# Performance work log

Measured on AMD Instinct MI355X. Metric: run time of the kernel, lower is better.

The kernel has to match this reference:

```python
import jax, jax.numpy as jnp
import numpy as np

B, T, D, H = 2, 2048, 2048, 16
HD = D // H
EPS = 1e-8
NEG = -1e9


def setup_inputs() -> dict:
    key = jax.random.key(0)
    ks = jax.random.split(key, 6)
    x = jax.random.normal(ks[0], (B, T, D), dtype=jnp.float32)
    # additive causal mask, broadcast over [B, H, T, T]
    causal = jnp.tril(jnp.ones((T, T), dtype=bool))
    attn_mask = jnp.where(causal, 0.0, NEG).astype(jnp.float32)[None, None]
    s = 1.0 / np.sqrt(D)
    w_norm = jnp.ones((D,), dtype=jnp.float32)
    wq = jax.random.normal(ks[1], (D, D), dtype=jnp.float32) * s
    wk = jax.random.normal(ks[2], (D, D), dtype=jnp.float32) * s
    wv = jax.random.normal(ks[3], (D, D), dtype=jnp.float32) * s
    wo = jax.random.normal(ks[4], (D, D), dtype=jnp.float32) * s
    return {"x": x, "attn_mask": attn_mask, "w_norm": w_norm,
            "wq": wq, "wk": wk, "wv": wv, "wo": wo}


def _rmsnorm(x, w):
    # norm = ||x||_2 * D^-0.5 ; out = w * x / (norm + eps)  (eps outside, as in source)
    norm = jnp.sqrt(jnp.sum(x * x, axis=-1, keepdims=True)) * (x.shape[-1] ** -0.5)
    return w * x / (norm + EPS)


def reference(x, attn_mask, w_norm, wq, wk, wv, wo):
    b, t, d = x.shape
    xn = _rmsnorm(x, w_norm)
    # Linear (no bias): y = x @ W^T ; split into heads -> [B, H, T, HD]
    def proj(w):
        return jnp.einsum('btd,ed->bte', xn, w).reshape(b, t, H, HD).transpose(0, 2, 1, 3)
    q, k, v = proj(wq), proj(wk), proj(wv)
    scale = HD ** -0.5
    w_scores = jnp.einsum('bhqd,bhkd->bhqk', q, k) * scale + attn_mask
    p = jax.nn.softmax(w_scores, axis=-1)
    out = jnp.einsum('bhqk,bhkd->bhqd', p, v)
    out = out.transpose(0, 2, 1, 3).reshape(b, t, d)
    return jnp.einsum('btd,ed->bte', out, wo)
```

## Files before the change

### kernel.cpp

```cpp
#include <hip/hip_runtime.h>
#include <stdint.h>

#define TT 2048
#define DD 2048
#define NHH 16
#define HDD 128
#define BTT 4096

typedef __attribute__((ext_vector_type(8))) short bf16x8;
typedef __attribute__((ext_vector_type(4))) float f32x4;

#define MF(a, b, c) __builtin_amdgcn_mfma_f32_16x16x32_bf16(a, b, c, 0, 0, 0)

__device__ __forceinline__ unsigned short f2bf(float f) {
    union { float f; uint32_t u; } v; v.f = f;
    uint32_t u = v.u;
    u += 0x7fffu + ((u >> 16) & 1u);
    return (unsigned short)(u >> 16);
}

__device__ __forceinline__ void gld16(const unsigned short* g, unsigned short* l) {
    __builtin_amdgcn_global_load_lds(
        (const __attribute__((address_space(1))) unsigned int*)g,
        (__attribute__((address_space(3))) unsigned int*)l, 16, 0, 0);
}

__global__ __launch_bounds__(256) void convert_w(const float* __restrict__ wq,
                                                 const float* __restrict__ wk,
                                                 const float* __restrict__ wv,
                                                 const float* __restrict__ wo,
                                                 unsigned short* __restrict__ out) {
    size_t gid = (size_t)blockIdx.x * 256 + threadIdx.x;
    size_t base = gid * 8;
    int which = (int)(base >> 22);
    const float* src = which == 0 ? wq : which == 1 ? wk : which == 2 ? wv : wo;
    size_t off = base & 4194303u;
    float4 a = ((const float4*)(src + off))[0];
    float4 b = ((const float4*)(src + off))[1];
    union { unsigned short us[8]; uint4 v; } pk;
    pk.us[0] = f2bf(a.x); pk.us[1] = f2bf(a.y); pk.us[2] = f2bf(a.z); pk.us[3] = f2bf(a.w);
    pk.us[4] = f2bf(b.x); pk.us[5] = f2bf(b.y); pk.us[6] = f2bf(b.z); pk.us[7] = f2bf(b.w);
    *(uint4*)(out + base) = pk.v;
}

__global__ __launch_bounds__(256) void rmsnorm_k(const float* __restrict__ x,
                                                 const float* __restrict__ w,
                                                 unsigned short* __restrict__ xn) {
    const int row = blockIdx.x;
    const int tid = threadIdx.x;
    const float* xr = x + (size_t)row * DD;
    float4 a = ((const float4*)xr)[tid * 2];
    float4 b = ((const float4*)xr)[tid * 2 + 1];
    float ss = a.x*a.x + a.y*a.y + a.z*a.z + a.w*a.w
             + b.x*b.x + b.y*b.y + b.z*b.z + b.w*b.w;
    #pragma unroll
    for (int m = 1; m < 64; m <<= 1) ss += __shfl_xor(ss, m, 64);
    __shared__ float wss[4];
    if ((tid & 63) == 0) wss[tid >> 6] = ss;
    __syncthreads();
    float total = wss[0] + wss[1] + wss[2] + wss[3];
    float norm = sqrtf(total) * 0.022097086912079612f;
    float inv = 1.0f / (norm + 1e-8f);
    float4 wa = ((const float4*)w)[tid * 2];
    float4 wb = ((const float4*)w)[tid * 2 + 1];
    union { unsigned short us[8]; uint4 v; } pk;
    pk.us[0] = f2bf(wa.x * a.x * inv); pk.us[1] = f2bf(wa.y * a.y * inv);
    pk.us[2] = f2bf(wa.z * a.z * inv); pk.us[3] = f2bf(wa.w * a.w * inv);
    pk.us[4] = f2bf(wb.x * b.x * inv); pk.us[5] = f2bf(wb.y * b.y * inv);
    pk.us[6] = f2bf(wb.z * b.z * inv); pk.us[7] = f2bf(wb.w * b.w * inv);
    ((uint4*)(xn + (size_t)row * DD))[tid] = pk.v;
}

__device__ __forceinline__ void stage_tile(const unsigned short* __restrict__ Ag,
                                           const unsigned short* __restrict__ Bg,
                                           int k0, unsigned short* buf,
                                           int swA, int swB, size_t goff) {
    #pragma unroll
    for (int c = 0; c < 2; c++)
        gld16(Ag + (size_t)(swA + c * 8) * DD + k0 + goff, buf + (swA + c * 8) * 64);
    #pragma unroll
    for (int c = 0; c < 4; c++)
        gld16(Bg + (size_t)(swB + c * 8) * DD + k0 + goff, buf + 8192 + (swB + c * 8) * 64);
}

__device__ __forceinline__ void gemm128x256_core(const unsigned short* __restrict__ Ag,
                                                 const unsigned short* __restrict__ Bg,
                                                 unsigned short* lds, f32x4 acc[4][4]) {
    const int tid = threadIdx.x;
    const int wave = tid >> 6, lane = tid & 63;
    const int wm = wave >> 2, wn = wave & 3;
    const int l15 = lane & 15, lq = lane >> 4, r7 = l15 & 7;
    const int gr = lane >> 3;
    const size_t goff = (size_t)gr * DD + (size_t)(((lane & 7) ^ gr) * 8);
    const int xk0 = (lq ^ r7) * 8;
    const int xk1 = ((4 + lq) ^ r7) * 8;
    const int aro = (wm * 64 + l15) * 64;
    const int bro = 8192 + (wn * 64 + l15) * 64;
    const int swA = wave * 16;
    const int swB = wave * 32;
    unsigned short* p0 = lds;
    unsigned short* p1 = lds + 24576;
    unsigned short* p2 = lds + 49152;

    stage_tile(Ag, Bg, 0, p0, swA, swB, goff);
    stage_tile(Ag, Bg, 64, p1, swA, swB, goff);
    asm volatile("s_waitcnt vmcnt(6)" ::: "memory");
    __builtin_amdgcn_sched_barrier(0);
    __builtin_amdgcn_s_barrier();

    for (int kt = 0; kt < 32; kt++) {
        if (kt + 2 < 32)
            stage_tile(Ag, Bg, (kt + 2) * 64, p2, swA, swB, goff);
        const unsigned short* ac = p0 + aro;
        const unsigned short* bc = p0 + bro;
        bf16x8 a[4][2], b[4][2];
        #pragma unroll
        for (int m = 0; m < 4; m++) {
            a[m][0] = *(const bf16x8*)(ac + m * 1024 + xk0);
            a[m][1] = *(const bf16x8*)(ac + m * 1024 + xk1);
        }
        #pragma unroll
        for (int n = 0; n < 4; n++) {
            b[n][0] = *(const bf16x8*)(bc + n * 1024 + xk0);
            b[n][1] = *(const bf16x8*)(bc + n * 1024 + xk1);
        }
        asm volatile("s_waitcnt lgkmcnt(0)" ::: "memory");
        __builtin_amdgcn_sched_barrier(0);
        __builtin_amdgcn_s_setprio(1);
        #pragma unroll
        for (int m = 0; m < 4; m++)
            #pragma unroll
            for (int n = 0; n < 4; n++) {
                acc[m][n] = MF(a[m][0], b[n][0], acc[m][n]);
                acc[m][n] = MF(a[m][1], b[n][1], acc[m][n]);
            }
        __builtin_amdgcn_s_setprio(0);
        if (kt + 1 < 32) {
            if (kt + 2 < 32) { asm volatile("s_waitcnt vmcnt(6)" ::: "memory"); }
            else             { asm volatile("s_waitcnt vmcnt(0)" ::: "memory"); }
            __builtin_amdgcn_sched_barrier(0);
        }
        __builtin_amdgcn_s_barrier();
        unsigned short* t = p0; p0 = p1; p1 = p2; p2 = t;
    }
}

__global__ __launch_bounds__(512, 2) void gemm_qkv(const unsigned short* __restrict__ A,
                                                   const unsigned short* __restrict__ W3,
                                                   unsigned short* __restrict__ O3) {
    __shared__ __align__(16) unsigned short lds[73728];
    const int orig = blockIdx.y * 32 + blockIdx.x;
    const int id = (orig & 7) * 96 + (orig >> 3);
    const int which = id >> 8;
    const int rem = id & 255;
    const int bn = rem >> 5, bm = rem & 31;
    const unsigned short* Bw = W3 + (size_t)which * DD * DD;
    unsigned short* C = O3 + (size_t)which * BTT * DD;
    const int m0 = bm * 128, n0 = bn * 256;
    const f32x4 zf = {0.f, 0.f, 0.f, 0.f};
    f32x4 acc[4][4];
    #pragma unroll
    for (int m = 0; m < 4; m++)
        #pragma unroll
        for (int n = 0; n < 4; n++) acc[m][n] = zf;
    gemm128x256_core(A + (size_t)m0 * DD, Bw + (size_t)n0 * DD, lds, acc);
    const int wave = threadIdx.x >> 6, lane = threadIdx.x & 63;
    const int wm = wave >> 2, wn = wave & 3;
    const int l15 = lane & 15, lq = lane >> 4;
    #pragma unroll
    for (int m = 0; m < 4; m++) {
        const int row = m0 + wm * 64 + m * 16 + lq * 4;
        #pragma unroll
        for (int n = 0; n < 4; n++) {
            const int col = n0 + wn * 64 + n * 16 + l15;
            #pragma unroll
            for (int r = 0; r < 4; r++)
                C[(size_t)(row + r) * DD + col] = f2bf(acc[m][n][r]);
        }
    }
}

__global__ __launch_bounds__(512, 2) void gemm_out(const unsigned short* __restrict__ A,
                                                   const unsigned short* __restrict__ Bw,
                                                   float* __restrict__ C) {
    __shared__ __align__(16) unsigned short lds[73728];
    const int orig = blockIdx.y * 32 + blockIdx.x;
    const int id = (orig & 7) * 32 + (orig >> 3);
    const int bn = id >> 5, bm = id & 31;
    const int m0 = bm * 128, n0 = bn * 256;
    const f32x4 zf = {0.f, 0.f, 0.f, 0.f};
    f32x4 acc[4][4];
    #pragma unroll
    for (int m = 0; m < 4; m++)
        #pragma unroll
        for (int n = 0; n < 4; n++) acc[m][n] = zf;
    gemm128x256_core(A + (size_t)m0 * DD, Bw + (size_t)n0 * DD, lds, acc);
    const int wave = threadIdx.x >> 6, lane = threadIdx.x & 63;
    const int wm = wave >> 2, wn = wave & 3;
    const int l15 = lane & 15, lq = lane >> 4;
    #pragma unroll
    for (int m = 0; m < 4; m++) {
        const int row = m0 + wm * 64 + m * 16 + lq * 4;
        #pragma unroll
        for (int n = 0; n < 4; n++) {
            const int col = n0 + wn * 64 + n * 16 + l15;
            #pragma unroll
            for (int r = 0; r < 4; r++)
                C[(size_t)(row + r) * DD + col] = acc[m][n][r];
        }
    }
}

__global__ __launch_bounds__(256) void attn_fused(const unsigned short* __restrict__ q,
                                                  const unsigned short* __restrict__ k,
                                                  const unsigned short* __restrict__ v,
                                                  unsigned short* __restrict__ o) {
    constexpr int LPP = 72;
    __shared__ __align__(16) unsigned short Ks[2][64 * 128];
    __shared__ __align__(16) unsigned short Vts[128 * 64];
    __shared__ __align__(16) unsigned short Ps[4 * 16 * LPP];
    const int h = blockIdx.y, b = blockIdx.z;
    const int tid = threadIdx.x, wave = tid >> 6, lane = tid & 63;
    const int l15 = lane & 15, lq = lane >> 4;
    const size_t rowbase = (size_t)b * TT;
    const int hcol = h * HDD;
    const float scale = 0.08838834764831845f;
    unsigned short* Pw = Ps + wave * 16 * LPP;
    const f32x4 zf = {0.f, 0.f, 0.f, 0.f};

    uint4 vr0, vr1, vr2, vr3;
    const int pr = tid >> 3;
    const int hc = (tid & 7) * 16;
    const int vsw0 = (2 * pr) ^ (((hc >> 3) & 7) << 3);
    const int vsw1 = (2 * pr) ^ ((((hc + 8) >> 3) & 7) << 3);

    const int klrow = lane >> 4;
    const int klch  = lane & 15;

    for (int half = 0; half < 2; half++) {
        const int qj = (half == 0) ? blockIdx.x : 31 - blockIdx.x;
        const int qt0 = qj * 64;
        bf16x8 aq[4];
        {
            const unsigned short* qrp = q + (rowbase + qt0 + wave * 16 + l15) * DD + hcol;
            #pragma unroll
            for (int kk = 0; kk < 4; kk++)
                aq[kk] = *(const bf16x8*)(qrp + kk * 32 + lq * 8);
        }
        f32x4 acc_o[8];
        #pragma unroll
        for (int jh = 0; jh < 8; jh++) acc_o[jh] = zf;
        float m_i[4], l_i[4];
        #pragma unroll
        for (int r = 0; r < 4; r++) { m_i[r] = -1e30f; l_i[r] = 0.f; }
        const int qp0 = qt0 + wave * 16 + lq * 4;
        const int nkt = qj + 1;

        __syncthreads();
        {
            const unsigned short* kg = k + rowbase * DD + hcol;
            const unsigned short* vg = v + rowbase * DD + hcol;
            #pragma unroll
            for (int i = 0; i < 4; i++) {
                const int r0 = wave * 16 + i * 4;
                const int row = r0 + klrow;
                const int gch = klch ^ (row & 7);
                gld16(kg + (size_t)row * DD + gch * 8, &Ks[0][r0 * 128]);
            }
            vr0 = *(const uint4*)(vg + (size_t)(2 * pr) * DD + hc);
            vr1 = *(const uint4*)(vg + (size_t)(2 * pr) * DD + hc + 8);
            vr2 = *(const uint4*)(vg + (size_t)(2 * pr + 1) * DD + hc);
            vr3 = *(const uint4*)(vg + (size_t)(2 * pr + 1) * DD + hc + 8);
        }

        for (int kt = 0; kt < nkt; kt++) {
            const int cur = kt & 1;
            __syncthreads();
            if (kt + 1 < nkt) {
                const unsigned short* kg = k + (rowbase + (kt + 1) * 64) * DD + hcol;
                #pragma unroll
                for (int i = 0; i < 4; i++) {
                    const int r0 = wave * 16 + i * 4;
                    const int row = r0 + klrow;
                    const int gch = klch ^ (row & 7);
                    gld16(kg + (size_t)row * DD + gch * 8, &Ks[cur ^ 1][r0 * 128]);
                }
            }
            {
                const unsigned short* s0 = (const unsigned short*)&vr0;
                const unsigned short* s1 = (const unsigned short*)&vr1;
                const unsigned short* s2 = (const unsigned short*)&vr2;
                const unsigned short* s3 = (const unsigned short*)&vr3;
                #pragma unroll
                for (int jj = 0; jj < 8; jj++) {
                    *(uint32_t*)(&Vts[(hc + jj) * 64 + vsw0]) =
                        (uint32_t)s0[jj] | ((uint32_t)s2[jj] << 16);
                    *(uint32_t*)(&Vts[(hc + 8 + jj) * 64 + vsw1]) =
                        (uint32_t)s1[jj] | ((uint32_t)s3[jj] << 16);
                }
            }
            if (kt + 1 < nkt) {
                const unsigned short* vg = v + (rowbase + (kt + 1) * 64) * DD + hcol;
                vr0 = *(const uint4*)(vg + (size_t)(2 * pr) * DD + hc);
                vr1 = *(const uint4*)(vg + (size_t)(2 * pr) * DD + hc + 8);
                vr2 = *(const uint4*)(vg + (size_t)(2 * pr + 1) * DD + hc);
                vr3 = *(const uint4*)(vg + (size_t)(2 * pr + 1) * DD + hc + 8);
            }
            const unsigned short* ksc = &Ks[cur][0];
            f32x4 accs[4];
            #pragma unroll
            for (int j = 0; j < 4; j++) accs[j] = zf;
            __builtin_amdgcn_s_setprio(1);
            #pragma unroll
            for (int j = 0; j < 4; j++)
                #pragma unroll
                for (int kk = 0; kk < 4; kk++) {
                    bf16x8 bk = *(const bf16x8*)(&ksc[(j * 16 + l15) * 128 +
                                                      (((kk * 4 + lq) ^ (l15 & 7)) * 8)]);
                    accs[j] = MF(aq[kk], bk, accs[j]);
                }
            __builtin_amdgcn_s_setprio(0);
            const int kbase = kt * 64;
            float rowmax[4] = {-1e30f, -1e30f, -1e30f, -1e30f};
            #pragma unroll
            for (int j = 0; j < 4; j++) {
                const int kp = kbase + j * 16 + l15;
                #pragma unroll
                for (int r = 0; r < 4; r++) {
                    float s = accs[j][r] * scale;
                    s = (kp > qp0 + r) ? -1e30f : s;
                    accs[j][r] = s;
                    rowmax[r] = fmaxf(rowmax[r], s);
                }
            }
            #pragma unroll
            for (int r = 0; r < 4; r++) {
                float mx = rowmax[r];
                mx = fmaxf(mx, __shfl_xor(mx, 1, 64));
                mx = fmaxf(mx, __shfl_xor(mx, 2, 64));
                mx = fmaxf(mx, __shfl_xor(mx, 4, 64));
                mx = fmaxf(mx, __shfl_xor(mx, 8, 64));
                float m_new = fmaxf(m_i[r], mx);
                float al = __expf(m_i[r] - m_new);
                m_i[r] = m_new;
                l_i[r] *= al;
                #pragma unroll
                for (int jh = 0; jh < 8; jh++) acc_o[jh][r] *= al;
            }
            float rowsum[4] = {0.f, 0.f, 0.f, 0.f};
            #pragma unroll
            for (int j = 0; j < 4; j++)
                #pragma unroll
                for (int r = 0; r < 4; r++) {
                    float p = __expf(accs[j][r] - m_i[r]);
                    rowsum[r] += p;
                    Pw[(lq * 4 + r) * LPP + j * 16 + l15] = f2bf(p);
                }
            #pragma unroll
            for (int r = 0; r < 4; r++) {
                float s = rowsum[r];
                s += __shfl_xor(s, 1, 64);
                s += __shfl_xor(s, 2, 64);
                s += __shfl_xor(s, 4, 64);
                s += __shfl_xor(s, 8, 64);
                l_i[r] += s;
            }
            __syncthreads();
            bf16x8 ap[2];
            #pragma unroll
            for (int kk = 0; kk < 2; kk++)
                ap[kk] = *(const bf16x8*)(&Pw[l15 * LPP + kk * 32 + lq * 8]);
            __builtin_amdgcn_s_setprio(1);
            #pragma unroll
            for (int jh = 0; jh < 8; jh++) {
                const int hd = jh * 16 + l15;
                const int vswz = ((hd >> 3) & 7) << 3;
                #pragma unroll
                for (int kk = 0; kk < 2; kk++) {
                    bf16x8 bv = *(const bf16x8*)(&Vts[hd * 64 + ((kk * 32 + lq * 8) ^ vswz)]);
                    acc_o[jh] = MF(ap[kk], bv, acc_o[jh]);
                }
            }
            __builtin_amdgcn_s_setprio(0);
        }
        #pragma unroll
        for (int jh = 0; jh < 8; jh++) {
            const int col = hcol + jh * 16 + l15;
            #pragma unroll
            for (int r = 0; r < 4; r++)
                o[(rowbase + qp0 + r) * DD + col] = f2bf(acc_o[jh][r] * (1.0f / l_i[r]));
        }
    }
}

extern "C" void kernel_launch(void* const* d_in, const int* in_sizes, int n_in,
                              void* d_out, int out_size, void* d_ws, size_t ws_size,
                              hipStream_t stream) {
    const float* x      = (const float*)d_in[0];
    const float* w_norm = (const float*)d_in[2];
    const float* wq     = (const float*)d_in[3];
    const float* wk     = (const float*)d_in[4];
    const float* wv     = (const float*)d_in[5];
    const float* wo     = (const float*)d_in[6];

    unsigned short* wbf = (unsigned short*)d_ws;
    unsigned short* xn  = wbf + (size_t)4 * DD * DD;
    unsigned short* qb  = xn + (size_t)BTT * DD;
    unsigned short* kb  = qb + (size_t)BTT * DD;
    unsigned short* vb  = kb + (size_t)BTT * DD;
    unsigned short* ab  = vb + (size_t)BTT * DD;

    convert_w<<<8192, 256, 0, stream>>>(wq, wk, wv, wo, wbf);
    rmsnorm_k<<<BTT, 256, 0, stream>>>(x, w_norm, xn);
    dim3 gqkv(32, 24);
    gemm_qkv<<<gqkv, 512, 0, stream>>>(xn, wbf, qb);
    dim3 gattn(16, NHH, 2);
    attn_fused<<<gattn, 256, 0, stream>>>(qb, kb, vb, ab);
    dim3 gout(32, 8);
    gemm_out<<<gout, 512, 0, stream>>>(ab, wbf + (size_t)3 * DD * DD, (float*)d_out);
}
```

Baseline: 412.4 us.

## Replace triple-buffered async LDS GEMM pipeline with register-staged double buffer, remap attention blocks

The GEMM core drops the direct global-to-LDS triple-buffered loads with 64-wide K tiles. In their place it loads 32-wide K slices into registers, computes on the current LDS buffer, then writes the registers into the other buffer. This shrinks LDS use from 144KB to 48KB per block and raises the launch-bounds occupancy hint from 2 to 4. It also remaps attention block indices so that consecutive blocks spread across batch/head groups, with the aim of better XCD or cache distribution. The cost is twice as many K iterations and barriers, plus extra VGPRs and LDS-write instructions.

```diff
diff --git a/kernel.cpp b/kernel.cpp
--- a/kernel.cpp
+++ b/kernel.cpp
@@ -71,84 +71,72 @@
     ((uint4*)(xn + (size_t)row * DD))[tid] = pk.v;
 }
 
-__device__ __forceinline__ void stage_tile(const unsigned short* __restrict__ Ag,
-                                           const unsigned short* __restrict__ Bg,
-                                           int k0, unsigned short* buf,
-                                           int swA, int swB, size_t goff) {
-    #pragma unroll
-    for (int c = 0; c < 2; c++)
-        gld16(Ag + (size_t)(swA + c * 8) * DD + k0 + goff, buf + (swA + c * 8) * 64);
-    #pragma unroll
-    for (int c = 0; c < 4; c++)
-        gld16(Bg + (size_t)(swB + c * 8) * DD + k0 + goff, buf + 8192 + (swB + c * 8) * 64);
-}
-
 __device__ __forceinline__ void gemm128x256_core(const unsigned short* __restrict__ Ag,
                                                  const unsigned short* __restrict__ Bg,
                                                  unsigned short* lds, f32x4 acc[4][4]) {
     const int tid = threadIdx.x;
     const int wave = tid >> 6, lane = tid & 63;
     const int wm = wave >> 2, wn = wave & 3;
-    const int l15 = lane & 15, lq = lane >> 4, r7 = l15 & 7;
-    const int gr = lane >> 3;
-    const size_t goff = (size_t)gr * DD + (size_t)(((lane & 7) ^ gr) * 8);
-    const int xk0 = (lq ^ r7) * 8;
-    const int xk1 = ((4 + lq) ^ r7) * 8;
-    const int aro = (wm * 64 + l15) * 64;
-    const int bro = 8192 + (wn * 64 + l15) * 64;
-    const int swA = wave * 16;
-    const int swB = wave * 32;
-    unsigned short* p0 = lds;
-    unsigned short* p1 = lds + 24576;
-    unsigned short* p2 = lds + 49152;
-
-    stage_tile(Ag, Bg, 0, p0, swA, swB, goff);
-    stage_tile(Ag, Bg, 64, p1, swA, swB, goff);
-    asm volatile("s_waitcnt vmcnt(6)" ::: "memory");
-    __builtin_amdgcn_sched_barrier(0);
+    const int l15 = lane & 15, lq = lane >> 4;
+    const unsigned short* ga  = Ag + (size_t)(wave * 16 + l15) * DD + lq * 8;
+    const unsigned short* gb0 = Bg + (size_t)(wave * 32 + l15) * DD + lq * 8;
+    const unsigned short* gb1 = Bg + (size_t)(wave * 32 + 16 + l15) * DD + lq * 8;
+    const int da  = wave * 512 + lane * 8;
+    const int db0 = 4096 + wave * 1024 + lane * 8;
+    const int db1 = 4096 + wave * 1024 + 512 + lane * 8;
+    const int ra = (wm * 4) * 512 + lq * 128 + l15 * 8;
+    const int rb = 4096 + (wn * 4) * 512 + lq * 128 + l15 * 8;
+
+    uint4 sA  = *(const uint4*)(ga);
+    uint4 sB0 = *(const uint4*)(gb0);
+    uint4 sB1 = *(const uint4*)(gb1);
+    *(uint4*)(lds + da)  = sA;
+    *(uint4*)(lds + db0) = sB0;
+    *(uint4*)(lds + db1) = sB1;
+    asm volatile("s_waitcnt lgkmcnt(0)" ::: "memory");
     __builtin_amdgcn_s_barrier();
 
-    for (int kt = 0; kt < 32; kt++) {
-        if (kt + 2 < 32)
-            stage_tile(Ag, Bg, (kt + 2) * 64, p2, swA, swB, goff);
-        const unsigned short* ac = p0 + aro;
-        const unsigned short* bc = p0 + bro;
-        bf16x8 a[4][2], b[4][2];
-        #pragma unroll
-        for (int m = 0; m < 4; m++) {
-            a[m][0] = *(const bf16x8*)(ac + m * 1024 + xk0);
-            a[m][1] = *(const bf16x8*)(ac + m * 1024 + xk1);
-        }
-        #pragma unroll
-        for (int n = 0; n < 4; n++) {
-            b[n][0] = *(const bf16x8*)(bc + n * 1024 + xk0);
-            b[n][1] = *(const bf16x8*)(bc + n * 1024 + xk1);
-        }
+    for (int kt = 0; kt < 64; kt++) {
+        const int cur = (kt & 1) ? 12288 : 0;
+        const int nxt = 12288 - cur;
+        if (kt + 1 < 64) {
+            const int ko = (kt + 1) * 32;
+            sA  = *(const uint4*)(ga + ko);
+            sB0 = *(const uint4*)(gb0 + ko);
+            sB1 = *(const uint4*)(gb1 + ko);
+            __builtin_amdgcn_sched_barrier(0);
+        }
+        const unsigned short* ac = lds + cur + ra;
+        const unsigned short* bc = lds + cur + rb;
+        bf16x8 a[4], b[4];
+        #pragma unroll
+        for (int i = 0; i < 4; i++) a[i] = *(const bf16x8*)(ac + i * 512);
+        #pragma unroll
+        for (int n = 0; n < 4; n++) b[n] = *(const bf16x8*)(bc + n * 512);
         asm volatile("s_waitcnt lgkmcnt(0)" ::: "memory");
         __builtin_amdgcn_sched_barrier(0);
         __builtin_amdgcn_s_setprio(1);
         #pragma unroll
-        for (int m = 0; m < 4; m++)
-            #pragma unroll
-            for (int n = 0; n < 4; n++) {
-                acc[m][n] = MF(a[m][0], b[n][0], acc[m][n]);
-                acc[m][n] = MF(a[m][1], b[n][1], acc[m][n]);
-            }
+        for (int i = 0; i < 4; i++)
+            #pragma unroll
+            for (int n = 0; n < 4; n++)
+                acc[i][n] = MF(a[i], b[n], acc[i][n]);
         __builtin_amdgcn_s_setprio(0);
-        if (kt + 1 < 32) {
-            if (kt + 2 < 32) { asm volatile("s_waitcnt vmcnt(6)" ::: "memory"); }
-            else             { asm volatile("s_waitcnt vmcnt(0)" ::: "memory"); }
+        if (kt + 1 < 64) {
+            *(uint4*)(lds + nxt + da)  = sA;
+            *(uint4*)(lds + nxt + db0) = sB0;
+            *(uint4*)(lds + nxt + db1) = sB1;
+            asm volatile("s_waitcnt lgkmcnt(0)" ::: "memory");
             __builtin_amdgcn_sched_barrier(0);
         }
         __builtin_amdgcn_s_barrier();
-        unsigned short* t = p0; p0 = p1; p1 = p2; p2 = t;
     }
 }
 
-__global__ __launch_bounds__(512, 2) void gemm_qkv(const unsigned short* __restrict__ A,
+__global__ __launch_bounds__(512, 4) void gemm_qkv(const unsigned short* __restrict__ A,
                                                    const unsigned short* __restrict__ W3,
                                                    unsigned short* __restrict__ O3) {
-    __shared__ __align__(16) unsigned short lds[73728];
+    __shared__ __align__(16) unsigned short lds[24576];
     const int orig = blockIdx.y * 32 + blockIdx.x;
     const int id = (orig & 7) * 96 + (orig >> 3);
     const int which = id >> 8;
@@ -180,10 +168,10 @@
     }
 }
 
-__global__ __launch_bounds__(512, 2) void gemm_out(const unsigned short* __restrict__ A,
+__global__ __launch_bounds__(512, 4) void gemm_out(const unsigned short* __restrict__ A,
                                                    const unsigned short* __restrict__ Bw,
                                                    float* __restrict__ C) {
-    __shared__ __align__(16) unsigned short lds[73728];
+    __shared__ __align__(16) unsigned short lds[24576];
     const int orig = blockIdx.y * 32 + blockIdx.x;
     const int id = (orig & 7) * 32 + (orig >> 3);
     const int bn = id >> 5, bm = id & 31;
@@ -219,7 +207,11 @@
     __shared__ __align__(16) unsigned short Ks[2][64 * 128];
     __shared__ __align__(16) unsigned short Vts[128 * 64];
     __shared__ __align__(16) unsigned short Ps[4 * 16 * LPP];
-    const int h = blockIdx.y, b = blockIdx.z;
+    const int lin = blockIdx.x + (blockIdx.y << 4) + (blockIdx.z << 8);
+    const int slot = lin >> 3;
+    const int g = ((lin & 7) << 2) + (slot >> 4);
+    const int pairi = slot & 15;
+    const int h = g & 15, b = g >> 4;
     const int tid = threadIdx.x, wave = tid >> 6, lane = tid & 63;
     const int l15 = lane & 15, lq = lane >> 4;
     const size_t rowbase = (size_t)b * TT;
@@ -238,7 +230,7 @@
     const int klch  = lane & 15;
 
     for (int half = 0; half < 2; half++) {
-        const int qj = (half == 0) ? blockIdx.x : 31 - blockIdx.x;
+        const int qj = (half == 0) ? pairi : 31 - pairi;
         const int qt0 = qj * 64;
         bf16x8 aq[4];
         {
```

Result: slower. 479.3 us (+16.2%).
